# Kernel tuning notes

Hardware: AMD Instinct MI355X
Metric: run time of the kernel (lower is better)

## Reference

```python
import jax, jax.numpy as jnp
import numpy as np
from jax import lax

EPS = 1e-5
OCC = 0.1
DN = ('NCDHW', 'OIDHW', 'NCDHW')


def _down_mask(m):
    # active-site dilation into the stride-2 output grid (kernel 3, stride 2, pad 1):
    # output voxel is active iff any input voxel in its receptive field is active.
    return lax.reduce_window(m, 0.0, lax.max, (1, 1, 3, 3, 3), (1, 1, 2, 2, 2),
                             [(0, 0), (0, 0), (1, 1), (1, 1), (1, 1)])


def _conv(x, w, s, p):
    return lax.conv_general_dilated(x, w, (s, s, s), [(p, p)] * 3, dimension_numbers=DN)


def _convT(x, w):
    # SparseInverseConv3d == stride-2 transposed conv restricted to the saved coords
    return lax.conv_transpose(x, w, (2, 2, 2), 'SAME', dimension_numbers=DN)


def _bn_relu(x, m):
    # BatchNorm1d over the ACTIVE voxels only (spconv applies BN to x.features of
    # shape [n_active, C]), then ReLU; inactive sites stay exactly zero.
    n = jnp.maximum(jnp.sum(m), 1.0)
    mu = jnp.sum(x * m, axis=(0, 2, 3, 4), keepdims=True) / n
    var = jnp.sum(jnp.square(x - mu) * m, axis=(0, 2, 3, 4), keepdims=True) / n
    return jax.nn.relu((x - mu) * lax.rsqrt(var + EPS)) * m


def _forward(x, mask, w_enc0, w_enc1, w_enc2, w_enc3, w_bt_down, w_bt_conv,
             w_up0, w_up1, w_up2, w_up3, w_fuse0, w_fuse1, w_fuse2, w_fuse3, w_final):
    m = [(mask < OCC).astype(x.dtype)]            # m[0]: 64^3 input active set (indice_key cp0)
    for _ in range(5):
        m.append(_down_mask(m[-1]))               # m[1..4]: cp1..cp3 outputs, m[5]: cp_bt output
    h = x * m[0]
    feats = []
    for i, w in enumerate((w_enc0, w_enc1, w_enc2, w_enc3)):
        h = _bn_relu(_conv(h, w, 2, 1), m[i + 1])  # SparseConv3d k3 s2 p1 + BN + ReLU
        feats.append(h)
    h = _bn_relu(_conv(h, w_bt_down, 2, 1), m[5])  # bottleneck_down
    h = _bn_relu(_conv(h, w_bt_conv, 1, 1), m[5])  # bottleneck SubMConv3d (same active set)
    ups = (w_up0, w_up1, w_up2, w_up3)
    fuses = (w_fuse0, w_fuse1, w_fuse2, w_fuse3)
    for i in range(4):
        mm = m[4 - i]
        h = _bn_relu(_convT(h, ups[i]), mm)        # SparseInverseConv3d + BN + ReLU
        h = jnp.concatenate([h, feats[3 - i]], axis=1)  # skip concat on features
        h = _bn_relu(_conv(h, fuses[i], 1, 0), mm)       # 1x1 SubM fuse + BN + ReLU
    return _bn_relu(_convT(h, w_final), m[0])      # final_up to full resolution


def setup_inputs() -> dict:
    key = jax.random.key(0)
    ks = jax.random.split(key, 20)
    G, Cin, Cout = 64, 8, 16
    chs = [64, 128, 256, 512]

    def w(k, co, ci, ksz):
        return jax.random.normal(k, (co, ci, ksz, ksz, ksz), jnp.float32) / np.float32(np.sqrt(ci * ksz ** 3))

    d = {}
    d['x'] = jax.random.normal(ks[0], (1, Cin, G, G, G), jnp.float32)
    d['mask'] = jax.random.uniform(ks[1], (1, 1, G, G, G), jnp.float32)
    ci = Cin
    for i, co in enumerate(chs):
        d[f'w_enc{i}'] = w(ks[2 + i], co, ci, 3)
        ci = co
    d['w_bt_down'] = w(ks[6], 1024, 512, 3)
    d['w_bt_conv'] = w(ks[7], 1024, 1024, 3)
    dec_in = [1024, 512, 256, 128]
    dec_out = [512, 256, 128, 64]
    for i in range(4):
        d[f'w_up{i}'] = w(ks[8 + i], dec_out[i], dec_in[i], 3)
        d[f'w_fuse{i}'] = w(ks[12 + i], dec_out[i], dec_out[i] * 2, 1)
    d['w_final'] = w(ks[16], Cout, 64, 3)
    return d


def reference(x, mask, w_enc0, w_enc1, w_enc2, w_enc3, w_bt_down, w_bt_conv,
              w_up0, w_up1, w_up2, w_up3, w_fuse0, w_fuse1, w_fuse2, w_fuse3, w_final):
    return _forward(x, mask, w_enc0, w_enc1, w_enc2, w_enc3, w_bt_down, w_bt_conv,
                    w_up0, w_up1, w_up2, w_up3, w_fuse0, w_fuse1, w_fuse2, w_fuse3, w_final)
```

## Files before the change

### kernel.cpp

```cpp
#include <hip/hip_runtime.h>
#include <hip/hip_bf16.h>

#define TPB 256

struct ParCfg { int zoff[9]; int kper[8]; };

__global__ __launch_bounds__(TPB) void k_mask0(const float* __restrict__ mask,
                                               float* __restrict__ m0, int n) {
  int i = blockIdx.x * TPB + threadIdx.x;
  if (i < n) m0[i] = (mask[i] < 0.1f) ? 1.0f : 0.0f;
}

__global__ __launch_bounds__(TPB) void k_downmask(const float* __restrict__ mi,
                                                  float* __restrict__ mo, int Dout) {
  int n = Dout * Dout * Dout;
  int idx = blockIdx.x * TPB + threadIdx.x;
  if (idx >= n) return;
  int Din = Dout * 2;
  int ox = idx % Dout, oy = (idx / Dout) % Dout, oz = idx / (Dout * Dout);
  float v = 0.f;
  for (int kz = 0; kz < 3; kz++) {
    int iz = 2 * oz + kz - 1; if ((unsigned)iz >= (unsigned)Din) continue;
    for (int ky = 0; ky < 3; ky++) {
      int iy = 2 * oy + ky - 1; if ((unsigned)iy >= (unsigned)Din) continue;
      for (int kx = 0; kx < 3; kx++) {
        int ix = 2 * ox + kx - 1; if ((unsigned)ix >= (unsigned)Din) continue;
        v = fmaxf(v, mi[(iz * Din + iy) * Din + ix]);
      }
    }
  }
  mo[idx] = v;
}

__global__ __launch_bounds__(TPB) void k_maskx(const float* __restrict__ x,
                                               const float* __restrict__ m,
                                               float* __restrict__ o,
                                               long total, int vox) {
  long i = blockIdx.x * (long)TPB + threadIdx.x;
  if (i < total) o[i] = x[i] * m[i % vox];
}

__global__ __launch_bounds__(TPB) void k_sumparts(const float* __restrict__ parts,
                                                  float* __restrict__ out,
                                                  long n, int s) {
  long i = blockIdx.x * (long)TPB + threadIdx.x;
  if (i >= n) return;
  float a = 0.f;
  for (int j = 0; j < s; j++) a += parts[(long)j * n + i];
  out[i] = a;
}

__global__ __launch_bounds__(TPB) void k_sumscat(const float* __restrict__ parts,
                                                 float* __restrict__ out,
                                                 int M, int Np, int Z, int Dh,
                                                 int lgDh, int cls) {
  long i = blockIdx.x * (long)TPB + threadIdx.x;
  long tot = (long)M * Np;
  if (i >= tot) return;
  int co = (int)(i >> (3 * lgDh));
  int pp = (int)(i & (Np - 1));
  float s = 0.f;
  for (int z = 0; z < Z; z++) s += parts[((long)z * M + co) * Np + pp];
  int px = cls & 1, py = (cls >> 1) & 1, pz = (cls >> 2) & 1;
  int ox = pp & (Dh - 1), oy = (pp >> lgDh) & (Dh - 1), oz = pp >> (2 * lgDh);
  int DF = Dh * 2;
  long fc = ((long)(2 * oz + pz) * DF + (2 * oy + py)) * DF + (2 * ox + px);
  out[(long)co * ((long)DF * DF * DF) + fc] = s;
}

__global__ __launch_bounds__(TPB) void k_sumscatA(const float* __restrict__ parts,
                                                  float* __restrict__ out,
                                                  int lgNp, int lgMN, int Dh,
                                                  int lgDh, ParCfg pc) {
  long idx = blockIdx.x * (long)TPB + threadIdx.x;
  if (idx >= (8L << lgMN)) return;
  int cls = (int)(idx >> lgMN);
  int r = (int)(idx & ((1L << lgMN) - 1));
  int co = r >> lgNp;
  int pp = r & ((1 << lgNp) - 1);
  float s = 0.f;
  for (int z = pc.zoff[cls]; z < pc.zoff[cls + 1]; z++)
    s += parts[((long)z << lgMN) + r];
  int px = cls & 1, py = (cls >> 1) & 1, pz = (cls >> 2) & 1;
  int ox = pp & (Dh - 1), oy = (pp >> lgDh) & (Dh - 1), oz = pp >> (2 * lgDh);
  int DF = Dh * 2;
  long fc = ((long)(2 * oz + pz) * DF + (2 * oy + py)) * DF + (2 * ox + px);
  out[(long)co * ((long)DF * DF * DF) + fc] = s;
}

__global__ __launch_bounds__(TPB) void k_bcol8(const float* __restrict__ in,
                                               float* __restrict__ Bcol,
                                               int K, int Din, int mode) {
  long idx = blockIdx.x * (long)TPB + threadIdx.x;
  if (idx >= (long)K * 8) return;
  int kg = (int)(idx >> 3), pp = (int)(idx & 7);
  int ci = kg / 27, tap = kg - ci * 27;
  int kz = tap / 9, r9 = tap - kz * 9;
  int ky = r9 / 3, kx = r9 - ky * 3;
  int oz = pp >> 2, oy = (pp >> 1) & 1, ox = pp & 1;
  int iz, iy, ix;
  if (mode == 0) { iz = 2 * oz + kz - 1; iy = 2 * oy + ky - 1; ix = 2 * ox + kx - 1; }
  else           { iz = oz + kz - 1;     iy = oy + ky - 1;     ix = ox + kx - 1; }
  float v = 0.f;
  if ((unsigned)iz < (unsigned)Din && (unsigned)iy < (unsigned)Din &&
      (unsigned)ix < (unsigned)Din)
    v = in[(long)ci * Din * Din * Din + ((long)iz * Din + iy) * Din + ix];
  Bcol[idx] = v;
}

__global__ __launch_bounds__(TPB) void k_gemv8d(const float* __restrict__ W,
                                                const float* __restrict__ Bcol,
                                                float* __restrict__ part,
                                                int M, int K, int kqPer) {
  const int t = threadIdx.x;
  const int co0 = blockIdx.x * 4;
  const int kq = K >> 2;
  int q0 = blockIdx.y * kqPer;
  int q1 = q0 + kqPer; if (q1 > kq) q1 = kq;
  float acc[4][8];
#pragma unroll
  for (int r = 0; r < 4; r++)
#pragma unroll
    for (int p = 0; p < 8; p++) acc[r][p] = 0.f;
  const float4* W4 = (const float4*)W;
  for (int i = q0 + t; i < q1; i += TPB) {
    float4 w4[4];
#pragma unroll
    for (int r = 0; r < 4; r++) w4[r] = W4[(long)(co0 + r) * kq + i];
    const float* bp = &Bcol[(long)i * 32];
#pragma unroll
    for (int j = 0; j < 4; j++) {
      const float4 b0 = *(const float4*)&bp[j * 8];
      const float4 b1 = *(const float4*)&bp[j * 8 + 4];
#pragma unroll
      for (int r = 0; r < 4; r++) {
        const float w = (j == 0) ? w4[r].x : (j == 1) ? w4[r].y
                        : (j == 2) ? w4[r].z : w4[r].w;
        acc[r][0] += w * b0.x; acc[r][1] += w * b0.y;
        acc[r][2] += w * b0.z; acc[r][3] += w * b0.w;
        acc[r][4] += w * b1.x; acc[r][5] += w * b1.y;
        acc[r][6] += w * b1.z; acc[r][7] += w * b1.w;
      }
    }
  }
#pragma unroll
  for (int off = 32; off > 0; off >>= 1)
#pragma unroll
    for (int r = 0; r < 4; r++)
#pragma unroll
      for (int p = 0; p < 8; p++) acc[r][p] += __shfl_down(acc[r][p], off);
  __shared__ float Rs[4][4][8];
  if ((t & 63) == 0) {
#pragma unroll
    for (int r = 0; r < 4; r++)
#pragma unroll
      for (int p = 0; p < 8; p++) Rs[t >> 6][r][p] = acc[r][p];
  }
  __syncthreads();
  if (t < 32) {
    int r = t >> 3, p = t & 7;
    part[((long)blockIdx.y * M + co0 + r) * 8 + p] =
        Rs[0][r][p] + Rs[1][r][p] + Rs[2][r][p] + Rs[3][r][p];
  }
}

template<int MT, int MODE>
__global__ __launch_bounds__(TPB) void k_gemm(const float* __restrict__ A,
                                              const float* __restrict__ B1,
                                              const float* __restrict__ B2,
                                              float* __restrict__ C,
                                              int M, int N, int K,
                                              int Din, int Dout, int C1,
                                              int kcPer) {
  constexpr int MR = MT / 16;
  constexpr int AEL = (MT == 64) ? 8 : 2;
  __shared__ __align__(16) float At[32][MT];
  __shared__ __align__(16) float Bt[32][64];

  const int t = threadIdx.x;
  const int n0 = blockIdx.x * 64;
  const int m0 = blockIdx.y * MT;

  const int p0 = (t & 15) * 4;
  const int co0 = (t >> 4) * MR;

  const int pb = t & 63;
  const int kb0 = (t >> 6) * 8;
  const int pp = n0 + pb;
  const int oxb = pp & (Dout - 1);
  const int oyb = (pp / Dout) & (Dout - 1);
  const int ozb = pp / (Dout * Dout);

  int px = 0, py = 0, pz = 0, lgnx = 0, lgny = 0, lgT = 0, Cin = 0;
  if (MODE == 4) {
    px = C1 & 1; py = (C1 >> 1) & 1; pz = (C1 >> 2) & 1;
    lgnx = 1 - px; lgny = 1 - py;
    lgT = lgnx + lgny + (1 - pz);
    Cin = K >> lgT;
  }

  const int nch = (K + 31) >> 5;
  const int c0 = blockIdx.z * kcPer;
  int c1 = c0 + kcPer; if (c1 > nch) c1 = nch;

  float acc[MR][4];
#pragma unroll
  for (int a = 0; a < MR; a++)
#pragma unroll
    for (int b = 0; b < 4; b++) acc[a][b] = 0.f;

  float raf[AEL];
  float rb[8];
  const int co_a = (MT == 64) ? (t >> 2) : (t & 15);
  const int ka   = (MT == 64) ? ((t & 3) * 8) : ((t >> 4) * 2);
  const long arow = (long)(m0 + co_a) * K;

  auto loadA = [&](int c) {
    const int k0 = c << 5;
    if (MODE == 4) {
#pragma unroll
      for (int j = 0; j < AEL; j++) {
        const int kg = k0 + ka + j;
        float v = 0.f;
        if (kg < K) {
          int ci = kg >> lgT;
          int tt = kg & ((1 << lgT) - 1);
          int tx = tt & ((1 << lgnx) - 1); tt >>= lgnx;
          int ty = tt & ((1 << lgny) - 1);
          int tz = tt >> lgny;
          int kx = px ? 1 : (tx << 1);
          int ky = py ? 1 : (ty << 1);
          int kz = pz ? 1 : (tz << 1);
          v = A[((long)(m0 + co_a) * Cin + ci) * 27 + (kz * 3 + ky) * 3 + kx];
        }
        raf[j] = v;
      }
    } else if (MT == 64) {
#pragma unroll
      for (int j = 0; j < 2; j++) {
        const int kg = k0 + ka + j * 4;
        float4 v = (kg < K) ? *(const float4*)&A[arow + kg]
                            : make_float4(0.f, 0.f, 0.f, 0.f);
        raf[j * 4 + 0] = v.x; raf[j * 4 + 1] = v.y;
        raf[j * 4 + 2] = v.z; raf[j * 4 + 3] = v.w;
      }
    } else {
      const int kg = k0 + ka;
      raf[0] = (kg < K) ? A[arow + kg] : 0.f;
      raf[1] = (kg + 1 < K) ? A[arow + kg + 1] : 0.f;
    }
  };

  auto loadB = [&](int c) {
    const int k0 = c << 5;
#pragma unroll
    for (int j = 0; j < 8; j++) {
      const int kg = k0 + kb0 + j;
      float v = 0.f;
      if (kg < K && pp < N) {
        if (MODE == 2) {
          v = (kg < C1) ? B1[(long)kg * N + pp] : B2[(long)(kg - C1) * N + pp];
        } else if (MODE == 4) {
          int ci = kg >> lgT;
          int tt = kg & ((1 << lgT) - 1);
          int tx = tt & ((1 << lgnx) - 1); tt >>= lgnx;
          int ty = tt & ((1 << lgny) - 1);
          int tz = tt >> lgny;
          int ix = px ? oxb : (oxb - 1 + tx);
          int iy = py ? oyb : (oyb - 1 + ty);
          int iz = pz ? ozb : (ozb - 1 + tz);
          if ((ix | iy | iz) >= 0)
            v = B1[(long)ci * Din * Din * Din + ((long)iz * Din + iy) * Din + ix];
        } else {
          const int ci = kg / 27;
          const int tap = kg - ci * 27;
          const int kz = tap / 9;
          const int r9 = tap - kz * 9;
          const int ky = r9 / 3;
          const int kx = r9 - ky * 3;
          int iz, iy, ix;
          bool ok;
          if (MODE == 0) {
            iz = 2 * ozb + kz - 1; iy = 2 * oyb + ky - 1; ix = 2 * oxb + kx - 1;
            ok = (unsigned)iz < (unsigned)Din && (unsigned)iy < (unsigned)Din &&
                 (unsigned)ix < (unsigned)Din;
          } else {
            iz = ozb + kz - 1; iy = oyb + ky - 1; ix = oxb + kx - 1;
            ok = (unsigned)iz < (unsigned)Din && (unsigned)iy < (unsigned)Din &&
                 (unsigned)ix < (unsigned)Din;
          }
          if (ok)
            v = B1[(long)ci * Din * Din * Din + ((long)iz * Din + iy) * Din + ix];
        }
      }
      rb[j] = v;
    }
  };

  if (c0 < c1) { loadA(c0); loadB(c0); }

  for (int c = c0; c < c1; ++c) {
    __syncthreads();
#pragma unroll
    for (int j = 0; j < AEL; j++) At[ka + j][co_a] = raf[j];
#pragma unroll
    for (int j = 0; j < 8; j++) Bt[kb0 + j][pb] = rb[j];
    if (c + 1 < c1) { loadA(c + 1); loadB(c + 1); }
    __syncthreads();
#pragma unroll
    for (int kk = 0; kk < 32; ++kk) {
      const float4 b4 = *(const float4*)&Bt[kk][p0];
      if (MR == 4) {
        const float4 a4 = *(const float4*)&At[kk][co0];
        acc[0][0] += a4.x * b4.x; acc[0][1] += a4.x * b4.y;
        acc[0][2] += a4.x * b4.z; acc[0][3] += a4.x * b4.w;
        acc[1][0] += a4.y * b4.x; acc[1][1] += a4.y * b4.y;
        acc[1][2] += a4.y * b4.z; acc[1][3] += a4.y * b4.w;
        acc[2][0] += a4.z * b4.x; acc[2][1] += a4.z * b4.y;
        acc[2][2] += a4.z * b4.z; acc[2][3] += a4.z * b4.w;
        acc[3][0] += a4.w * b4.x; acc[3][1] += a4.w * b4.y;
        acc[3][2] += a4.w * b4.z; acc[3][3] += a4.w * b4.w;
      } else {
        const float a = At[kk][co0];
        acc[0][0] += a * b4.x; acc[0][1] += a * b4.y;
        acc[0][2] += a * b4.z; acc[0][3] += a * b4.w;
      }
    }
  }

  if (MODE == 4 && gridDim.z == 1) {
    const int lgD = 31 - __clz(Dout);
    const int DF = Din << 1;
    const long voxF = (long)DF * DF * DF;
#pragma unroll
    for (int mr = 0; mr < MR; mr++) {
#pragma unroll
      for (int e = 0; e < 4; e++) {
        int pp2 = n0 + p0 + e;
        if (pp2 < N) {
          int ox = pp2 & (Dout - 1), oy = (pp2 >> lgD) & (Dout - 1),
              oz = pp2 >> (2 * lgD);
          long fc = ((long)(2 * oz + pz) * DF + (2 * oy + py)) * DF +
                    (2 * ox + px);
          C[(long)(m0 + co0 + mr) * voxF + fc] = acc[mr][e];
        }
      }
    }
  } else {
    float* Cz = C + (long)blockIdx.z * ((long)M * N);
#pragma unroll
    for (int mr = 0; mr < MR; mr++) {
      if (n0 + p0 < N) {
        float4 v = make_float4(acc[mr][0], acc[mr][1], acc[mr][2], acc[mr][3]);
        *(float4*)&Cz[(long)(m0 + co0 + mr) * N + n0 + p0] = v;
      }
    }
  }
}

template<int MT>
__global__ __launch_bounds__(TPB) void k_gemmTm(const float* __restrict__ A,
                                                const float* __restrict__ B1,
                                                float* __restrict__ C,
                                                int M, int N, int Cin, int Din,
                                                ParCfg pc, int direct) {
  constexpr int MR = MT / 16;
  constexpr int AEL = (MT == 64) ? 8 : 2;
  __shared__ __align__(16) float At[32][MT];
  __shared__ __align__(16) float Bt[32][64];

  const int t = threadIdx.x;
  const int n0 = blockIdx.x * 64;
  const int m0 = blockIdx.y * MT;
  const int z = blockIdx.z;

  int cls = 0;
#pragma unroll
  for (int c = 1; c < 8; c++) if (z >= pc.zoff[c]) cls = c;
  const int zi = z - pc.zoff[cls];
  const int kperc = pc.kper[cls];

  const int px = cls & 1, py = (cls >> 1) & 1, pz = (cls >> 2) & 1;
  const int lgnx = 1 - px, lgny = 1 - py;
  const int lgT = lgnx + lgny + (1 - pz);
  const int K = Cin << lgT;
  const int nch = K >> 5;

  const int p0 = (t & 15) * 4;
  const int co0 = (t >> 4) * MR;
  const int pb = t & 63;
  const int kb0 = (t >> 6) * 8;
  const int pp = n0 + pb;
  const int oxb = pp & (Din - 1);
  const int oyb = (pp / Din) & (Din - 1);
  const int ozb = pp / (Din * Din);

  const int c0 = zi * kperc;
  int c1 = c0 + kperc; if (c1 > nch) c1 = nch;

  float acc[MR][4];
#pragma unroll
  for (int a = 0; a < MR; a++)
#pragma unroll
    for (int b = 0; b < 4; b++) acc[a][b] = 0.f;

  float raf[AEL];
  float rb[8];
  const int co_a = (MT == 64) ? (t >> 2) : (t & 15);
  const int ka   = (MT == 64) ? ((t & 3) * 8) : ((t >> 4) * 2);

  auto loadA = [&](int c) {
    const int k0 = c << 5;
#pragma unroll
    for (int j = 0; j < AEL; j++) {
      const int kg = k0 + ka + j;
      float v = 0.f;
      if (kg < K) {
        int ci = kg >> lgT;
        int tt = kg & ((1 << lgT) - 1);
        int tx = tt & ((1 << lgnx) - 1); tt >>= lgnx;
        int ty = tt & ((1 << lgny) - 1);
        int tz = tt >> lgny;
        int kx = px ? 1 : (tx << 1);
        int ky = py ? 1 : (ty << 1);
        int kz = pz ? 1 : (tz << 1);
        v = A[((long)(m0 + co_a) * Cin + ci) * 27 + (kz * 3 + ky) * 3 + kx];
      }
      raf[j] = v;
    }
  };

  auto loadB = [&](int c) {
    const int k0 = c << 5;
#pragma unroll
    for (int j = 0; j < 8; j++) {
      const int kg = k0 + kb0 + j;
      float v = 0.f;
      if (kg < K && pp < N) {
        int ci = kg >> lgT;
        int tt = kg & ((1 << lgT) - 1);
        int tx = tt & ((1 << lgnx) - 1); tt >>= lgnx;
        int ty = tt & ((1 << lgny) - 1);
        int tz = tt >> lgny;
        int ix = px ? oxb : (oxb - 1 + tx);
        int iy = py ? oyb : (oyb - 1 + ty);
        int iz = pz ? ozb : (ozb - 1 + tz);
        if ((ix | iy | iz) >= 0)
          v = B1[(long)ci * Din * Din * Din + ((long)iz * Din + iy) * Din + ix];
      }
      rb[j] = v;
    }
  };

  if (c0 < c1) { loadA(c0); loadB(c0); }

  for (int c = c0; c < c1; ++c) {
    __syncthreads();
#pragma unroll
    for (int j = 0; j < AEL; j++) At[ka + j][co_a] = raf[j];
#pragma unroll
    for (int j = 0; j < 8; j++) Bt[kb0 + j][pb] = rb[j];
    if (c + 1 < c1) { loadA(c + 1); loadB(c + 1); }
    __syncthreads();
#pragma unroll
    for (int kk = 0; kk < 32; ++kk) {
      const float4 b4 = *(const float4*)&Bt[kk][p0];
      if (MR == 4) {
        const float4 a4 = *(const float4*)&At[kk][co0];
        acc[0][0] += a4.x * b4.x; acc[0][1] += a4.x * b4.y;
        acc[0][2] += a4.x * b4.z; acc[0][3] += a4.x * b4.w;
        acc[1][0] += a4.y * b4.x; acc[1][1] += a4.y * b4.y;
        acc[1][2] += a4.y * b4.z; acc[1][3] += a4.y * b4.w;
        acc[2][0] += a4.z * b4.x; acc[2][1] += a4.z * b4.y;
        acc[2][2] += a4.z * b4.z; acc[2][3] += a4.z * b4.w;
        acc[3][0] += a4.w * b4.x; acc[3][1] += a4.w * b4.y;
        acc[3][2] += a4.w * b4.z; acc[3][3] += a4.w * b4.w;
      } else {
        const float a = At[kk][co0];
        acc[0][0] += a * b4.x; acc[0][1] += a * b4.y;
        acc[0][2] += a * b4.z; acc[0][3] += a * b4.w;
      }
    }
  }

  if (direct) {
    const int lgD = 31 - __clz(Din);
    const int DF = Din << 1;
    const long voxF = (long)DF * DF * DF;
#pragma unroll
    for (int mr = 0; mr < MR; mr++) {
#pragma unroll
      for (int e = 0; e < 4; e++) {
        int pp2 = n0 + p0 + e;
        if (pp2 < N) {
          int ox = pp2 & (Din - 1), oy = (pp2 >> lgD) & (Din - 1),
              oz = pp2 >> (2 * lgD);
          long fc = ((long)(2 * oz + pz) * DF + (2 * oy + py)) * DF +
                    (2 * ox + px);
          C[(long)(m0 + co0 + mr) * voxF + fc] = acc[mr][e];
        }
      }
    }
  } else {
    float* Cz = C + (long)z * ((long)M * N);
#pragma unroll
    for (int mr = 0; mr < MR; mr++) {
      if (n0 + p0 < N) {
        float4 v = make_float4(acc[mr][0], acc[mr][1], acc[mr][2], acc[mr][3]);
        *(float4*)&Cz[(long)(m0 + co0 + mr) * N + n0 + p0] = v;
      }
    }
  }
}

__global__ __launch_bounds__(TPB) void k_stats1(const float* __restrict__ a,
                                                const float* __restrict__ m,
                                                float* __restrict__ part,
                                                float* __restrict__ partM,
                                                int vox, int chunk) {
  const int s = blockIdx.x, c = blockIdx.y;
  const float* ap = a + (long)c * vox + (long)s * chunk;
  const float* mp = m + (long)s * chunk;
  float s0 = 0.f, s1 = 0.f, sm = 0.f;
  for (int i = threadIdx.x; i < chunk; i += TPB) {
    float mv = mp[i];
    float v = ap[i] * mv;
    s0 += v; s1 += v * v; sm += mv;
  }
  __shared__ float sh0[TPB], sh1[TPB], sh2[TPB];
  sh0[threadIdx.x] = s0; sh1[threadIdx.x] = s1; sh2[threadIdx.x] = sm;
  __syncthreads();
  for (int off = TPB / 2; off > 0; off >>= 1) {
    if (threadIdx.x < off) {
      sh0[threadIdx.x] += sh0[threadIdx.x + off];
      sh1[threadIdx.x] += sh1[threadIdx.x + off];
      sh2[threadIdx.x] += sh2[threadIdx.x + off];
    }
    __syncthreads();
  }
  if (threadIdx.x == 0) {
    const int S = gridDim.x;
    part[(c * S + s) * 2] = sh0[0];
    part[(c * S + s) * 2 + 1] = sh1[0];
    if (c == 0) partM[s] = sh2[0];
  }
}

__global__ __launch_bounds__(64) void k_stats2(const float* __restrict__ part,
                                               const float* __restrict__ partM,
                                               float* __restrict__ stats, int S) {
  const int c = blockIdx.x, t = threadIdx.x;
  float s0 = 0.f, s1 = 0.f, sm = 0.f;
  for (int s = t; s < S; s += 64) {
    s0 += part[(c * S + s) * 2];
    s1 += part[(c * S + s) * 2 + 1];
    sm += partM[s];
  }
  for (int off = 32; off > 0; off >>= 1) {
    s0 += __shfl_down(s0, off);
    s1 += __shfl_down(s1, off);
    sm += __shfl_down(sm, off);
  }
  if (t == 0) {
    float n = fmaxf(sm, 1.f);
    float mu = s0 / n;
    float var = fmaxf(s1 / n - mu * mu, 0.f);
    stats[2 * c] = mu;
    stats[2 * c + 1] = rsqrtf(var + 1e-5f);
  }
}

__global__ __launch_bounds__(TPB) void k_apply(float* __restrict__ a,
                                               const float* __restrict__ m,
                                               const float* __restrict__ stats,
                                               int vox, long total) {
  long idx = blockIdx.x * (long)TPB + threadIdx.x;
  if (idx >= total) return;
  int c = (int)(idx / vox);
  int p = (int)(idx % vox);
  float v = (a[idx] - stats[2 * c]) * stats[2 * c + 1];
  a[idx] = fmaxf(v, 0.f) * m[p];
}

__global__ __launch_bounds__(TPB) void k_apply_out(const float* __restrict__ a,
                                                   const float* __restrict__ m,
                                                   const float* __restrict__ stats,
                                                   float* __restrict__ out,
                                                   int vox, long total) {
  long idx = blockIdx.x * (long)TPB + threadIdx.x;
  if (idx >= total) return;
  int c = (int)(idx / vox);
  int p = (int)(idx % vox);
  float v = (a[idx] - stats[2 * c]) * stats[2 * c + 1];
  out[idx] = fmaxf(v, 0.f) * m[p];
}

constexpr long o_m0 = 0;
constexpr long o_m1 = 262144;
constexpr long o_m2 = 294912;
constexpr long o_m3 = 299008;
constexpr long o_m4 = 299520;
constexpr long o_m5 = 299584;
constexpr long o_st = 299592;
constexpr long o_A  = 301696;
constexpr long o_B  = 2398848;
constexpr long o_C  = 4496000;
constexpr long o_D  = 5020288;
constexpr long o_E  = 5151360;
constexpr long o_F  = 5184128;
constexpr long o_G  = 5192320;
constexpr long o_H  = 5200512;
constexpr long o_I  = 5233280;
constexpr long o_J  = 5266048;
constexpr long o_K  = 5397120;
constexpr long o_L  = 5528192;
constexpr long o_M  = 6052480;
constexpr long o_N  = 6576768;
constexpr long o_P  = 8673920;
constexpr long o_PM = 8690304;
constexpr long o_fin = o_A;

extern "C" void kernel_launch(void* const* d_in, const int* in_sizes, int n_in,
                              void* d_out, int out_size, void* d_ws, size_t ws_size,
                              hipStream_t stream) {
  const float* x      = (const float*)d_in[0];
  const float* mask   = (const float*)d_in[1];
  const float* w_enc0 = (const float*)d_in[2];
  const float* w_enc1 = (const float*)d_in[3];
  const float* w_enc2 = (const float*)d_in[4];
  const float* w_enc3 = (const float*)d_in[5];
  const float* w_btd  = (const float*)d_in[6];
  const float* w_btc  = (const float*)d_in[7];
  const float* w_up0  = (const float*)d_in[8];
  const float* w_fu0  = (const float*)d_in[9];
  const float* w_up1  = (const float*)d_in[10];
  const float* w_fu1  = (const float*)d_in[11];
  const float* w_up2  = (const float*)d_in[12];
  const float* w_fu2  = (const float*)d_in[13];
  const float* w_up3  = (const float*)d_in[14];
  const float* w_fu3  = (const float*)d_in[15];
  const float* w_fin  = (const float*)d_in[16];

  float* ws = (float*)d_ws;
  float* st = ws + o_st;
  float* out = (float*)d_out;

  auto blocks = [](long n) { return (unsigned)((n + TPB - 1) / TPB); };

  k_mask0<<<blocks(262144), TPB, 0, stream>>>(mask, ws + o_m0, 262144);
  k_downmask<<<blocks(32768), TPB, 0, stream>>>(ws + o_m0, ws + o_m1, 32);
  k_downmask<<<blocks(4096), TPB, 0, stream>>>(ws + o_m1, ws + o_m2, 16);
  k_downmask<<<blocks(512), TPB, 0, stream>>>(ws + o_m2, ws + o_m3, 8);
  k_downmask<<<blocks(64), TPB, 0, stream>>>(ws + o_m3, ws + o_m4, 4);
  k_downmask<<<blocks(8), TPB, 0, stream>>>(ws + o_m4, ws + o_m5, 2);

  k_maskx<<<blocks(8L * 262144), TPB, 0, stream>>>(x, ws + o_m0, ws + o_A,
                                                   8L * 262144, 262144);

  auto stats = [&](const float* a, const float* m, int C, int vox) {
    int S = vox / TPB; if (S < 1) S = 1; if (S > 64) S = 64;
    int chunk = vox / S;
    dim3 g(S, C);
    k_stats1<<<g, TPB, 0, stream>>>(a, m, ws + o_P, ws + o_PM, vox, chunk);
    k_stats2<<<C, 64, 0, stream>>>(ws + o_P, ws + o_PM, st, S);
  };
  auto bnrelu = [&](float* a, const float* m, int C, int vox) {
    stats(a, m, C, vox);
    long total = (long)C * vox;
    k_apply<<<blocks(total), TPB, 0, stream>>>(a, m, st, vox, total);
  };

#define GEMM(MT, MODE, A_, B1_, B2_, O_, M_, N_, K_, DIN_, DOUT_, C1_, Z_)   \
  do {                                                                        \
    int nch_ = ((K_) + 31) >> 5;                                              \
    int kper_ = (nch_ + (Z_) - 1) / (Z_);                                     \
    dim3 g_(((N_) + 63) / 64, (M_) / (MT), (Z_));                             \
    float* dst_ = ((Z_) > 1) ? (ws + o_A) : (O_);                             \
    k_gemm<MT, MODE><<<g_, TPB, 0, stream>>>(A_, B1_, B2_, dst_, M_, N_, K_,  \
                                             DIN_, DOUT_, C1_, kper_);        \
    if ((Z_) > 1)                                                             \
      k_sumparts<<<blocks((long)(M_) * (N_)), TPB, 0, stream>>>(              \
          ws + o_A, O_, (long)(M_) * (N_), (Z_));                             \
  } while (0)

  auto convTmerged = [&](const float* w, const float* in, float* o, int M,
                         int Cin, int Dh, int d) {
    int lgDh = 31 - __builtin_clz(Dh);
    int Np = Dh * Dh * Dh;
    ParCfg pc;
    int acc = 0;
    for (int c = 0; c < 8; c++) {
      pc.zoff[c] = acc;
      int px = c & 1, py = (c >> 1) & 1, pz = (c >> 2) & 1;
      int T = 1 << ((1 - px) + (1 - py) + (1 - pz));
      int nch = (Cin * T) >> 5;
      pc.kper[c] = d;
      acc += (nch + d - 1) / d;
    }
    pc.zoff[8] = acc;
    dim3 g((Np + 63) / 64, M / 64, acc);
    k_gemmTm<64><<<g, TPB, 0, stream>>>(w, in, ws + o_A, M, Np, Cin, Dh, pc, 0);
    int lgNp = 3 * lgDh;
    int lgMN = lgNp + (31 - __builtin_clz(M));
    k_sumscatA<<<blocks(8L << lgMN), TPB, 0, stream>>>(ws + o_A, o, lgNp, lgMN,
                                                       Dh, lgDh, pc);
  };

  auto convTpar = [&](const float* w, const float* in, float* o, int M, int Cin,
                      int Dh, float* scr, long scrCap) {
    int lgDh = 31 - __builtin_clz(Dh);
    int Np = Dh * Dh * Dh;
    for (int cls = 0; cls < 8; ++cls) {
      int px = cls & 1, py = (cls >> 1) & 1, pz = (cls >> 2) & 1;
      int T = 1 << ((1 - px) + (1 - py) + (1 - pz));
      int K = Cin * T;
      int nch = (K + 31) >> 5;
      long cap = scrCap / ((long)M * Np);
      int Z = nch; if (Z > cap) Z = (int)cap; if (Z > 128) Z = 128;
      if (Z < 1) Z = 1;
      int kper = (nch + Z - 1) / Z;
      dim3 g((Np + 63) / 64, M / 64, Z);
      if (Z == 1) {
        k_gemm<64, 4><<<g, TPB, 0, stream>>>(w, in, nullptr, o, M, Np, K,
                                             Dh, Dh, cls, kper);
      } else {
        k_gemm<64, 4><<<g, TPB, 0, stream>>>(w, in, nullptr, scr, M, Np, K,
                                             Dh, Dh, cls, kper);
        k_sumscat<<<blocks((long)M * Np), TPB, 0, stream>>>(scr, o, M, Np, Z,
                                                            Dh, lgDh, cls);
      }
    }
  };

  auto gemv8 = [&](const float* w, const float* in, float* o, int M, int Cin,
                   int Din, int mode, int Z) {
    int K = Cin * 27;
    float* bcol = ws + o_A;
    float* parts = ws + o_A + 262144;
    k_bcol8<<<blocks((long)K * 8), TPB, 0, stream>>>(in, bcol, K, Din, mode);
    int kq = K >> 2;
    int kqPer = (kq + Z - 1) / Z;
    dim3 g(M / 4, Z);
    k_gemv8d<<<g, TPB, 0, stream>>>(w, bcol, parts, M, K, kqPer);
    k_sumparts<<<blocks((long)M * 8), TPB, 0, stream>>>(parts, o, (long)M * 8, Z);
  };

  GEMM(64, 0, w_enc0, ws + o_A, nullptr, ws + o_B, 64, 32768, 8 * 27, 64, 32, 0, 1);
  bnrelu(ws + o_B, ws + o_m1, 64, 32768);
  GEMM(64, 0, w_enc1, ws + o_B, nullptr, ws + o_C, 128, 4096, 64 * 27, 32, 16, 0, 4);
  bnrelu(ws + o_C, ws + o_m2, 128, 4096);
  GEMM(64, 0, w_enc2, ws + o_C, nullptr, ws + o_D, 256, 512, 128 * 27, 16, 8, 0, 16);
  bnrelu(ws + o_D, ws + o_m3, 256, 512);
  GEMM(64, 0, w_enc3, ws + o_D, nullptr, ws + o_E, 512, 64, 256 * 27, 8, 4, 0, 64);
  bnrelu(ws + o_E, ws + o_m4, 512, 64);

  gemv8(w_btd, ws + o_E, ws + o_F, 1024, 512, 4, 0, 4);
  bnrelu(ws + o_F, ws + o_m5, 1024, 8);
  gemv8(w_btc, ws + o_F, ws + o_G, 1024, 1024, 2, 3, 4);
  bnrelu(ws + o_G, ws + o_m5, 1024, 8);

  convTmerged(w_up0, ws + o_G, ws + o_H, 512, 1024, 2, 4);
  bnrelu(ws + o_H, ws + o_m4, 512, 64);
  GEMM(64, 2, w_fu0, ws + o_H, ws + o_E, ws + o_I, 512, 64, 1024, 4, 4, 512, 32);
  bnrelu(ws + o_I, ws + o_m4, 512, 64);

  convTmerged(w_up1, ws + o_I, ws + o_J, 256, 512, 4, 4);
  bnrelu(ws + o_J, ws + o_m3, 256, 512);
  GEMM(64, 2, w_fu1, ws + o_J, ws + o_D, ws + o_K, 256, 512, 512, 8, 8, 256, 16);
  bnrelu(ws + o_K, ws + o_m3, 256, 512);

  convTmerged(w_up2, ws + o_K, ws + o_L, 128, 256, 8, 8);
  bnrelu(ws + o_L, ws + o_m2, 128, 4096);
  GEMM(64, 2, w_fu2, ws + o_L, ws + o_C, ws + o_M, 128, 4096, 256, 16, 16, 128, 2);
  bnrelu(ws + o_M, ws + o_m2, 128, 4096);

  convTpar(w_up3, ws + o_M, ws + o_A, 64, 128, 16, ws + o_N, 2097152);
  bnrelu(ws + o_A, ws + o_m1, 64, 32768);
  GEMM(64, 2, w_fu3, ws + o_A, ws + o_B, ws + o_N, 64, 32768, 128, 32, 32, 64, 1);
  bnrelu(ws + o_N, ws + o_m1, 64, 32768);

  {
    ParCfg pc;
    for (int c = 0; c < 8; c++) {
      pc.zoff[c] = c;
      int px = c & 1, py = (c >> 1) & 1, pz = (c >> 2) & 1;
      int T = 1 << ((1 - px) + (1 - py) + (1 - pz));
      pc.kper[c] = (64 * T) >> 5;
    }
    pc.zoff[8] = 8;
    dim3 g(32768 / 64, 1, 8);
    k_gemmTm<16><<<g, TPB, 0, stream>>>(w_fin, ws + o_N, ws + o_fin,
                                        16, 32768, 64, 32, pc, 1);
  }
  {
    int vox = 262144, C = 16;
    int S = 64, chunk = vox / S;
    dim3 g(S, C);
    k_stats1<<<g, TPB, 0, stream>>>(ws + o_fin, ws + o_m0, ws + o_P, ws + o_PM,
                                    vox, chunk);
    k_stats2<<<C, 64, 0, stream>>>(ws + o_P, ws + o_PM, st, S);
    long total = (long)C * vox;
    k_apply_out<<<blocks(total), TPB, 0, stream>>>(ws + o_fin, ws + o_m0, st,
                                                   out, vox, total);
  }
#undef GEMM
}
```

Measured before the change: 884.0 us.

## Merge last transposed conv into one launch and add dedicated final upsample kernel

The last decoder transposed conv (up3) used to launch eight separate per-parity-class GEMMs, each followed by a scatter-sum. It now goes through the merged single-launch gemmTm path with a split-K depth of 32 and one sumscatA reduction. The final 64->16 transposed conv replaces the tiled gemmTm<16> with a new k_finup kernel. In k_finup each thread owns one voxel, computes all 16 output channels, and reads the class weights from shared memory. The change removes launch overhead and poor tile utilisation, at the cost of a scratch-buffer round trip for up3 and less load coalescing control in the new kernel.

```diff
diff --git a/kernel.cpp b/kernel.cpp
--- a/kernel.cpp
+++ b/kernel.cpp
@@ -48,24 +48,6 @@
   float a = 0.f;
   for (int j = 0; j < s; j++) a += parts[(long)j * n + i];
   out[i] = a;
-}
-
-__global__ __launch_bounds__(TPB) void k_sumscat(const float* __restrict__ parts,
-                                                 float* __restrict__ out,
-                                                 int M, int Np, int Z, int Dh,
-                                                 int lgDh, int cls) {
-  long i = blockIdx.x * (long)TPB + threadIdx.x;
-  long tot = (long)M * Np;
-  if (i >= tot) return;
-  int co = (int)(i >> (3 * lgDh));
-  int pp = (int)(i & (Np - 1));
-  float s = 0.f;
-  for (int z = 0; z < Z; z++) s += parts[((long)z * M + co) * Np + pp];
-  int px = cls & 1, py = (cls >> 1) & 1, pz = (cls >> 2) & 1;
-  int ox = pp & (Dh - 1), oy = (pp >> lgDh) & (Dh - 1), oz = pp >> (2 * lgDh);
-  int DF = Dh * 2;
-  long fc = ((long)(2 * oz + pz) * DF + (2 * oy + py)) * DF + (2 * ox + px);
-  out[(long)co * ((long)DF * DF * DF) + fc] = s;
 }
 
 __global__ __launch_bounds__(TPB) void k_sumscatA(const float* __restrict__ parts,
@@ -191,14 +173,6 @@
   const int oyb = (pp / Dout) & (Dout - 1);
   const int ozb = pp / (Dout * Dout);
 
-  int px = 0, py = 0, pz = 0, lgnx = 0, lgny = 0, lgT = 0, Cin = 0;
-  if (MODE == 4) {
-    px = C1 & 1; py = (C1 >> 1) & 1; pz = (C1 >> 2) & 1;
-    lgnx = 1 - px; lgny = 1 - py;
-    lgT = lgnx + lgny + (1 - pz);
-    Cin = K >> lgT;
-  }
-
   const int nch = (K + 31) >> 5;
   const int c0 = blockIdx.z * kcPer;
   int c1 = c0 + kcPer; if (c1 > nch) c1 = nch;
@@ -217,25 +191,7 @@
 
   auto loadA = [&](int c) {
     const int k0 = c << 5;
-    if (MODE == 4) {
-#pragma unroll
-      for (int j = 0; j < AEL; j++) {
-        const int kg = k0 + ka + j;
-        float v = 0.f;
-        if (kg < K) {
-          int ci = kg >> lgT;
-          int tt = kg & ((1 << lgT) - 1);
-          int tx = tt & ((1 << lgnx) - 1); tt >>= lgnx;
-          int ty = tt & ((1 << lgny) - 1);
-          int tz = tt >> lgny;
-          int kx = px ? 1 : (tx << 1);
-          int ky = py ? 1 : (ty << 1);
-          int kz = pz ? 1 : (tz << 1);
-          v = A[((long)(m0 + co_a) * Cin + ci) * 27 + (kz * 3 + ky) * 3 + kx];
-        }
-        raf[j] = v;
-      }
-    } else if (MT == 64) {
+    if (MT == 64) {
 #pragma unroll
       for (int j = 0; j < 2; j++) {
         const int kg = k0 + ka + j * 4;
@@ -260,17 +216,6 @@
       if (kg < K && pp < N) {
         if (MODE == 2) {
           v = (kg < C1) ? B1[(long)kg * N + pp] : B2[(long)(kg - C1) * N + pp];
-        } else if (MODE == 4) {
-          int ci = kg >> lgT;
-          int tt = kg & ((1 << lgT) - 1);
-          int tx = tt & ((1 << lgnx) - 1); tt >>= lgnx;
-          int ty = tt & ((1 << lgny) - 1);
-          int tz = tt >> lgny;
-          int ix = px ? oxb : (oxb - 1 + tx);
-          int iy = py ? oyb : (oyb - 1 + ty);
-          int iz = pz ? ozb : (ozb - 1 + tz);
-          if ((ix | iy | iz) >= 0)
-            v = B1[(long)ci * Din * Din * Din + ((long)iz * Din + iy) * Din + ix];
         } else {
           const int ci = kg / 27;
           const int tap = kg - ci * 27;
@@ -328,32 +273,12 @@
     }
   }
 
-  if (MODE == 4 && gridDim.z == 1) {
-    const int lgD = 31 - __clz(Dout);
-    const int DF = Din << 1;
-    const long voxF = (long)DF * DF * DF;
-#pragma unroll
-    for (int mr = 0; mr < MR; mr++) {
-#pragma unroll
-      for (int e = 0; e < 4; e++) {
-        int pp2 = n0 + p0 + e;
-        if (pp2 < N) {
-          int ox = pp2 & (Dout - 1), oy = (pp2 >> lgD) & (Dout - 1),
-              oz = pp2 >> (2 * lgD);
-          long fc = ((long)(2 * oz + pz) * DF + (2 * oy + py)) * DF +
-                    (2 * ox + px);
-          C[(long)(m0 + co0 + mr) * voxF + fc] = acc[mr][e];
-        }
-      }
-    }
-  } else {
-    float* Cz = C + (long)blockIdx.z * ((long)M * N);
-#pragma unroll
-    for (int mr = 0; mr < MR; mr++) {
-      if (n0 + p0 < N) {
-        float4 v = make_float4(acc[mr][0], acc[mr][1], acc[mr][2], acc[mr][3]);
-        *(float4*)&Cz[(long)(m0 + co0 + mr) * N + n0 + p0] = v;
-      }
+  float* Cz = C + (long)blockIdx.z * ((long)M * N);
+#pragma unroll
+  for (int mr = 0; mr < MR; mr++) {
+    if (n0 + p0 < N) {
+      float4 v = make_float4(acc[mr][0], acc[mr][1], acc[mr][2], acc[mr][3]);
+      *(float4*)&Cz[(long)(m0 + co0 + mr) * N + n0 + p0] = v;
     }
   }
 }
@@ -363,7 +288,7 @@
                                                 const float* __restrict__ B1,
                                                 float* __restrict__ C,
                                                 int M, int N, int Cin, int Din,
-                                                ParCfg pc, int direct) {
+                                                ParCfg pc) {
   constexpr int MR = MT / 16;
   constexpr int AEL = (MT == 64) ? 8 : 2;
   __shared__ __align__(16) float At[32][MT];
@@ -483,34 +408,87 @@
     }
   }
 
-  if (direct) {
-    const int lgD = 31 - __clz(Din);
-    const int DF = Din << 1;
-    const long voxF = (long)DF * DF * DF;
-#pragma unroll
-    for (int mr = 0; mr < MR; mr++) {
-#pragma unroll
-      for (int e = 0; e < 4; e++) {
-        int pp2 = n0 + p0 + e;
-        if (pp2 < N) {
-          int ox = pp2 & (Din - 1), oy = (pp2 >> lgD) & (Din - 1),
-              oz = pp2 >> (2 * lgD);
-          long fc = ((long)(2 * oz + pz) * DF + (2 * oy + py)) * DF +
-                    (2 * ox + px);
-          C[(long)(m0 + co0 + mr) * voxF + fc] = acc[mr][e];
+  float* Cz = C + (long)z * ((long)M * N);
+#pragma unroll
+  for (int mr = 0; mr < MR; mr++) {
+    if (n0 + p0 < N) {
+      float4 v = make_float4(acc[mr][0], acc[mr][1], acc[mr][2], acc[mr][3]);
+      *(float4*)&Cz[(long)(m0 + co0 + mr) * N + n0 + p0] = v;
+    }
+  }
+}
+
+__global__ __launch_bounds__(TPB) void k_finup(const float* __restrict__ A,
+                                               const float* __restrict__ B1,
+                                               float* __restrict__ C) {
+  __shared__ __align__(16) float Ws[8192];
+  const int cls = blockIdx.z;
+  const int px = cls & 1, py = (cls >> 1) & 1, pz = (cls >> 2) & 1;
+  const int lgnx = 1 - px, lgny = 1 - py;
+  const int lgT = lgnx + lgny + (1 - pz);
+  const int T = 1 << lgT;
+  const int K = 64 << lgT;
+
+  for (int idx = threadIdx.x; idx < K * 16; idx += TPB) {
+    int k = idx >> 4, co = idx & 15;
+    int ci = k >> lgT;
+    int tt = k & (T - 1);
+    int tx = tt & ((1 << lgnx) - 1);
+    int r = tt >> lgnx;
+    int ty = r & ((1 << lgny) - 1);
+    int tz = r >> lgny;
+    int kx = px ? 1 : (tx << 1);
+    int ky = py ? 1 : (ty << 1);
+    int kz = pz ? 1 : (tz << 1);
+    Ws[idx] = A[((long)co * 64 + ci) * 27 + (kz * 3 + ky) * 3 + kx];
+  }
+
+  const int pp = blockIdx.x * TPB + threadIdx.x;
+  const int oxb = pp & 31, oyb = (pp >> 5) & 31, ozb = pp >> 10;
+  const int bz = ozb - 1 + pz, by = oyb - 1 + py, bx = oxb - 1 + px;
+  const long laneOff = (long)bz * 1024 + by * 32 + bx;
+  unsigned vmask = 0;
+  {
+    int nz_ = pz ? 1 : 2, ny_ = py ? 1 : 2, nx_ = px ? 1 : 2;
+    for (int tz = 0; tz < nz_; tz++)
+      for (int ty = 0; ty < ny_; ty++)
+        for (int tx = 0; tx < nx_; tx++) {
+          bool ok = (unsigned)(bz + tz) < 32u && (unsigned)(by + ty) < 32u &&
+                    (unsigned)(bx + tx) < 32u;
+          if (ok) vmask |= 1u << ((tz << (lgny + lgnx)) | (ty << lgnx) | tx);
         }
-      }
-    }
-  } else {
-    float* Cz = C + (long)z * ((long)M * N);
-#pragma unroll
-    for (int mr = 0; mr < MR; mr++) {
-      if (n0 + p0 < N) {
-        float4 v = make_float4(acc[mr][0], acc[mr][1], acc[mr][2], acc[mr][3]);
-        *(float4*)&Cz[(long)(m0 + co0 + mr) * N + n0 + p0] = v;
-      }
-    }
-  }
+  }
+  __syncthreads();
+
+  float acc[16];
+#pragma unroll
+  for (int co = 0; co < 16; co++) acc[co] = 0.f;
+
+  for (int k = 0; k < K; k++) {
+    int ci = k >> lgT;
+    int tt = k & (T - 1);
+    int tx = tt & ((1 << lgnx) - 1);
+    int r = tt >> lgnx;
+    int ty = r & ((1 << lgny) - 1);
+    int tz = r >> lgny;
+    float b = 0.f;
+    if ((vmask >> tt) & 1)
+      b = B1[(long)ci * 32768 + (long)tz * 1024 + ty * 32 + tx + laneOff];
+    const float4* wp = (const float4*)&Ws[k * 16];
+#pragma unroll
+    for (int q = 0; q < 4; q++) {
+      float4 w = wp[q];
+      acc[q * 4 + 0] += w.x * b;
+      acc[q * 4 + 1] += w.y * b;
+      acc[q * 4 + 2] += w.z * b;
+      acc[q * 4 + 3] += w.w * b;
+    }
+  }
+
+  const long fc = ((long)(2 * ozb + pz) * 64 + (2 * oyb + py)) * 64 +
+                  (2 * oxb + px);
+#pragma unroll
+  for (int co = 0; co < 16; co++) C[(long)co * 262144 + fc] = acc[co];
 }
 
 __global__ __launch_bounds__(TPB) void k_stats1(const float* __restrict__ a,
@@ -684,7 +662,7 @@
   } while (0)
 
   auto convTmerged = [&](const float* w, const float* in, float* o, int M,
-                         int Cin, int Dh, int d) {
+                         int Cin, int Dh, int d, float* scr) {
     int lgDh = 31 - __builtin_clz(Dh);
     int Np = Dh * Dh * Dh;
     ParCfg pc;
@@ -699,37 +677,11 @@
     }
     pc.zoff[8] = acc;
     dim3 g((Np + 63) / 64, M / 64, acc);
-    k_gemmTm<64><<<g, TPB, 0, stream>>>(w, in, ws + o_A, M, Np, Cin, Dh, pc, 0);
+    k_gemmTm<64><<<g, TPB, 0, stream>>>(w, in, scr, M, Np, Cin, Dh, pc);
     int lgNp = 3 * lgDh;
     int lgMN = lgNp + (31 - __builtin_clz(M));
-    k_sumscatA<<<blocks(8L << lgMN), TPB, 0, stream>>>(ws + o_A, o, lgNp, lgMN,
+    k_sumscatA<<<blocks(8L << lgMN), TPB, 0, stream>>>(scr, o, lgNp, lgMN,
                                                        Dh, lgDh, pc);
-  };
-
-  auto convTpar = [&](const float* w, const float* in, float* o, int M, int Cin,
-                      int Dh, float* scr, long scrCap) {
-    int lgDh = 31 - __builtin_clz(Dh);
-    int Np = Dh * Dh * Dh;
-    for (int cls = 0; cls < 8; ++cls) {
-      int px = cls & 1, py = (cls >> 1) & 1, pz = (cls >> 2) & 1;
-      int T = 1 << ((1 - px) + (1 - py) + (1 - pz));
-      int K = Cin * T;
-      int nch = (K + 31) >> 5;
-      long cap = scrCap / ((long)M * Np);
-      int Z = nch; if (Z > cap) Z = (int)cap; if (Z > 128) Z = 128;
-      if (Z < 1) Z = 1;
-      int kper = (nch + Z - 1) / Z;
-      dim3 g((Np + 63) / 64, M / 64, Z);
-      if (Z == 1) {
-        k_gemm<64, 4><<<g, TPB, 0, stream>>>(w, in, nullptr, o, M, Np, K,
-                                             Dh, Dh, cls, kper);
-      } else {
-        k_gemm<64, 4><<<g, TPB, 0, stream>>>(w, in, nullptr, scr, M, Np, K,
-                                             Dh, Dh, cls, kper);
-        k_sumscat<<<blocks((long)M * Np), TPB, 0, stream>>>(scr, o, M, Np, Z,
-                                                            Dh, lgDh, cls);
-      }
-    }
   };
 
   auto gemv8 = [&](const float* w, const float* in, float* o, int M, int Cin,
@@ -759,38 +711,29 @@
   gemv8(w_btc, ws + o_F, ws + o_G, 1024, 1024, 2, 3, 4);
   bnrelu(ws + o_G, ws + o_m5, 1024, 8);
 
-  convTmerged(w_up0, ws + o_G, ws + o_H, 512, 1024, 2, 4);
+  convTmerged(w_up0, ws + o_G, ws + o_H, 512, 1024, 2, 4, ws + o_A);
   bnrelu(ws + o_H, ws + o_m4, 512, 64);
   GEMM(64, 2, w_fu0, ws + o_H, ws + o_E, ws + o_I, 512, 64, 1024, 4, 4, 512, 32);
   bnrelu(ws + o_I, ws + o_m4, 512, 64);
 
-  convTmerged(w_up1, ws + o_I, ws + o_J, 256, 512, 4, 4);
+  convTmerged(w_up1, ws + o_I, ws + o_J, 256, 512, 4, 4, ws + o_A);
   bnrelu(ws + o_J, ws + o_m3, 256, 512);
   GEMM(64, 2, w_fu1, ws + o_J, ws + o_D, ws + o_K, 256, 512, 512, 8, 8, 256, 16);
   bnrelu(ws + o_K, ws + o_m3, 256, 512);
 
-  convTmerged(w_up2, ws + o_K, ws + o_L, 128, 256, 8, 8);
+  convTmerged(w_up2, ws + o_K, ws + o_L, 128, 256, 8, 8, ws + o_A);
   bnrelu(ws + o_L, ws + o_m2, 128, 4096);
   GEMM(64, 2, w_fu2, ws + o_L, ws + o_C, ws + o_M, 128, 4096, 256, 16, 16, 128, 2);
   bnrelu(ws + o_M, ws + o_m2, 128, 4096);
 
-  convTpar(w_up3, ws + o_M, ws + o_A, 64, 128, 16, ws + o_N, 2097152);
+  convTmerged(w_up3, ws + o_M, ws + o_A, 64, 128, 16, 32, ws + o_N);
   bnrelu(ws + o_A, ws + o_m1, 64, 32768);
   GEMM(64, 2, w_fu3, ws + o_A, ws + o_B, ws + o_N, 64, 32768, 128, 32, 32, 64, 1);
   bnrelu(ws + o_N, ws + o_m1, 64, 32768);
 
   {
-    ParCfg pc;
-    for (int c = 0; c < 8; c++) {
-      pc.zoff[c] = c;
-      int px = c & 1, py = (c >> 1) & 1, pz = (c >> 2) & 1;
-      int T = 1 << ((1 - px) + (1 - py) + (1 - pz));
-      pc.kper[c] = (64 * T) >> 5;
-    }
-    pc.zoff[8] = 8;
-    dim3 g(32768 / 64, 1, 8);
-    k_gemmTm<16><<<g, TPB, 0, stream>>>(w_fin, ws + o_N, ws + o_fin,
-                                        16, 32768, 64, 32, pc, 1);
+    dim3 g(32768 / TPB, 1, 8);
+    k_finup<<<g, TPB, 0, stream>>>(w_fin, ws + o_N, ws + o_fin);
   }
   {
     int vox = 262144, C = 16;
```

New measurement: 834.5 us. -5.6%, faster.
